# Performance work log

Hardware: AMD Instinct MI355X
Metric: run time of the kernel (lower is better)

## Reference

```python
import jax, jax.numpy as jnp
import numpy as np

B, S, D, H = 2, 2048, 128, 8  # batch, seq, num_hidden(=head dim), num_heads
EPS = 1e-5


def setup_inputs() -> dict:
    key = jax.random.key(0)
    ks = jax.random.split(key, 12)
    sc = 0.02
    return {
        "query": jax.random.normal(ks[0], (B, S, D), dtype=jnp.float32),
        "Wq": jax.random.normal(ks[1], (2 * H * D, D), dtype=jnp.float32) * sc,
        "bq": jnp.zeros((2 * H * D,), dtype=jnp.float32),
        "Wk": jax.random.normal(ks[2], (2 * H * D, D), dtype=jnp.float32) * sc,
        "bk": jnp.zeros((2 * H * D,), dtype=jnp.float32),
        "Wv": jax.random.normal(ks[3], (H * D, D), dtype=jnp.float32) * sc,
        "bv": jnp.zeros((H * D,), dtype=jnp.float32),
        "Wo": jax.random.normal(ks[4], (D, H * D), dtype=jnp.float32) * sc,
        "bo": jnp.zeros((D,), dtype=jnp.float32),
        "gn_w": jnp.ones((H,), dtype=jnp.float32),
        "gn_b": jnp.zeros((H,), dtype=jnp.float32),
        "lam": jax.random.uniform(ks[5], (), dtype=jnp.float32),
    }


def reference(query, Wq, bq, Wk, bk, Wv, bv, Wo, bo, gn_w, gn_b, lam):
    # Faithful to the torch module: the .view calls are raw reshapes (no
    # transpose), d_k=1 so scale is 1, mask=None path (no causal mask),
    # dropout in eval mode, _lambda == _lambda_init == lam.
    q = (query @ Wq.T + bq).reshape(B, H, S, 2 * D)
    k = (query @ Wk.T + bk).reshape(B, H, S, 2 * D)
    v = (query @ Wv.T + bv).reshape(B, H, S, D)
    q1, q2 = q[..., :D], q[..., D:]
    k1, k2 = k[..., :D], k[..., D:]
    s1 = jnp.einsum("bhqd,bhkd->bhqk", q1, k1)  # / sqrt(d_k=1)
    s2 = jnp.einsum("bhqd,bhkd->bhqk", q2, k2)
    attn = jax.nn.softmax(s1, axis=-1) - lam * jax.nn.softmax(s2, axis=-1)
    out = jnp.einsum("bhqk,bhkd->bhqd", attn, v)          # (B,H,S,D)
    out = out.transpose(0, 2, 1, 3).reshape(B, H, S, D)   # faithful raw reshape
    # GroupNorm(num_groups=H, num_channels=H): normalize per (b, h) over (S, D)
    mean = out.mean(axis=(2, 3), keepdims=True)
    var = out.var(axis=(2, 3), keepdims=True)
    out = (out - mean) * jax.lax.rsqrt(var + EPS)
    out = out * gn_w[None, :, None, None] + gn_b[None, :, None, None]
    out = out * (1.0 - lam)
    # torch.cat([out[:, i] for i in range(H)], dim=-1) -> (B, S, H*D)
    out = out.transpose(0, 2, 1, 3).reshape(B, S, H * D)
    return out @ Wo.T + bo
```

## Files before the change

kernel.cpp:

```cpp
#include <hip/hip_runtime.h>

typedef __bf16 bf16x8 __attribute__((ext_vector_type(8)));
typedef __bf16 bf16x4 __attribute__((ext_vector_type(4)));
typedef float  f32x4  __attribute__((ext_vector_type(4)));

#define MFMA16(a,b,c) __builtin_amdgcn_mfma_f32_16x16x32_bf16((a),(b),(c),0,0,0)

__device__ __forceinline__ bf16x8 cvt8(float4 a, float4 b) {
  bf16x8 v;
  v[0]=(__bf16)a.x; v[1]=(__bf16)a.y; v[2]=(__bf16)a.z; v[3]=(__bf16)a.w;
  v[4]=(__bf16)b.x; v[5]=(__bf16)b.y; v[6]=(__bf16)b.z; v[7]=(__bf16)b.w;
  return v;
}
__device__ __forceinline__ bf16x4 cvt4(float4 a) {
  bf16x4 v;
  v[0]=(__bf16)a.x; v[1]=(__bf16)a.y; v[2]=(__bf16)a.z; v[3]=(__bf16)a.w;
  return v;
}


__global__ void to_bf16(const float* __restrict__ q,  const float* __restrict__ wq,
                        const float* __restrict__ wk, const float* __restrict__ wv,
                        const float* __restrict__ wo,
                        __bf16* __restrict__ qb,  __bf16* __restrict__ wqb,
                        __bf16* __restrict__ wkb, __bf16* __restrict__ wvb,
                        __bf16* __restrict__ wob)
{
  const long e = (long)(blockIdx.x * 256 + threadIdx.x) * 8;
  const float* src; __bf16* dst; long off;
  if (e < 524288)       { src = q;  dst = qb;  off = e; }
  else if (e < 786432)  { src = wq; dst = wqb; off = e - 524288; }
  else if (e < 1048576) { src = wk; dst = wkb; off = e - 786432; }
  else if (e < 1179648) { src = wv; dst = wvb; off = e - 1048576; }
  else                  { src = wo; dst = wob; off = e - 1179648; }
  *(bf16x8*)(dst + off) = cvt8(*(const float4*)(src + off), *(const float4*)(src + off + 4));
}

#define LDA 136
__global__ __launch_bounds__(256, 2) void qkv_gemm(
    const __bf16* __restrict__ queryb,
    const __bf16* __restrict__ Wqb, const float* __restrict__ bq,
    const __bf16* __restrict__ Wkb, const float* __restrict__ bk,
    const __bf16* __restrict__ Wvb, const float* __restrict__ bv,
    __bf16* __restrict__ Qbf, __bf16* __restrict__ Kbf, __bf16* __restrict__ Vt)
{
  __shared__ __bf16 As[128 * LDA];
  __shared__ __bf16 Bs[128 * LDA];
  const int t = threadIdx.x;
  const int tile = blockIdx.x;
  const int tm = tile / 40, tn = tile % 40;
  const int m0 = tm * 128, n0 = tn * 128;

  const __bf16* wbase; const float* bias;
  int ocol0; float oscale; int omode;
  if (n0 < 2048)      { wbase = Wqb + n0*128;        bias = bq + n0;        ocol0 = n0;      oscale = 1.4426950408889634f; omode = 0; }
  else if (n0 < 4096) { wbase = Wkb + (n0-2048)*128; bias = bk + (n0-2048); ocol0 = n0-2048; oscale = 1.0f; omode = 1; }
  else                { wbase = Wvb + (n0-4096)*128; bias = bv + (n0-4096); ocol0 = n0-4096; oscale = 1.0f; omode = 2; }

  const __bf16* abase = queryb + (long)m0 * 128;
  for (int r = 0; r < 2; ++r) {
    int e = (r*256 + t) * 32;
    int row = e >> 7, col = e & 127;
    #pragma unroll
    for (int c = 0; c < 4; ++c) {
      *(bf16x8*)&As[row*LDA + col + c*8] = *(const bf16x8*)(abase + (long)row*128 + col + c*8);
      *(bf16x8*)&Bs[row*LDA + col + c*8] = *(const bf16x8*)(wbase + (long)row*128 + col + c*8);
    }
  }
  __syncthreads();

  const int w = t >> 6, lane = t & 63;
  const int lo = lane & 15, quad = lane >> 4;
  const int wm = w >> 1, wn = w & 1;

  f32x4 acc[4][4];
  #pragma unroll
  for (int i = 0; i < 4; ++i)
    #pragma unroll
    for (int j = 0; j < 4; ++j) acc[i][j] = (f32x4){0.f,0.f,0.f,0.f};

  #pragma unroll
  for (int ks = 0; ks < 4; ++ks) {
    bf16x8 af[4], bfr[4];
    #pragma unroll
    for (int i = 0; i < 4; ++i)
      af[i] = *(const bf16x8*)&As[(wm*64 + i*16 + lo)*LDA + ks*32 + quad*8];
    #pragma unroll
    for (int j = 0; j < 4; ++j)
      bfr[j] = *(const bf16x8*)&Bs[(wn*64 + j*16 + lo)*LDA + ks*32 + quad*8];
    #pragma unroll
    for (int i = 0; i < 4; ++i)
      #pragma unroll
      for (int j = 0; j < 4; ++j)
        acc[i][j] = MFMA16(bfr[j], af[i], acc[i][j]);
  }

  if (omode == 2) {
    __syncthreads();
    #pragma unroll
    for (int j = 0; j < 4; ++j) {
      const f32x4 b4 = *(const f32x4*)(bias + wn*64 + j*16 + quad*4);
      #pragma unroll
      for (int i = 0; i < 4; ++i) {
        const int p_l = wm*64 + i*16 + lo;
        #pragma unroll
        for (int r = 0; r < 4; ++r) {
          const int dd_l = wn*64 + j*16 + quad*4 + r;
          As[dd_l*LDA + p_l] = (__bf16)(acc[i][j][r] + b4[r]);
        }
      }
    }
    __syncthreads();
    const int chunkV = ocol0 >> 7;
    __bf16* dst = Vt + (long)(m0 >> 8)*262144 + chunkV*256 + (m0 & 255);
    for (int rr = 0; rr < 8; ++rr) {
      const int unit = rr*256 + t;
      const int dd = unit >> 4, s8 = unit & 15;
      bf16x8 v = *(const bf16x8*)&As[dd*LDA + s8*8];
      *(bf16x8*)(dst + (long)dd*2048 + s8*8) = v;
    }
    return;
  }

  #pragma unroll
  for (int j = 0; j < 4; ++j) {
    const int colb = ocol0 + wn*64 + j*16 + quad*4;
    const f32x4 b4 = *(const f32x4*)(bias + wn*64 + j*16 + quad*4);
    #pragma unroll
    for (int i = 0; i < 4; ++i) {
      const int row = m0 + wm*64 + i*16 + lo;
      bf16x4 v;
      #pragma unroll
      for (int r = 0; r < 4; ++r) v[r] = (__bf16)((acc[i][j][r] + b4[r]) * oscale);
      if (omode == 1) {
        const long flat = (long)(row >> 8)*524288 + (long)(colb >> 8)*65536
                        + (row & 255)*256 + (colb & 255);
        *(bf16x4*)&Kbf[flat] = v;
      } else {
        *(bf16x4*)&Qbf[(long)row*2048 + colb] = v;
      }
    }
  }
}

__global__ __launch_bounds__(256, 2) void attn(
    const __bf16* __restrict__ Qbf, const __bf16* __restrict__ Kbf,
    const __bf16* __restrict__ Vt, __bf16* __restrict__ O,
    const float* __restrict__ lam_p, float* __restrict__ stats)
{
  __shared__ __align__(16) char pool[57344];
  __bf16* Ks  = (__bf16*)pool;
  __bf16* Vs  = (__bf16*)(pool + 32768);
  float*  red = (float*)(pool + 49152);

  const int t = threadIdx.x;
  const int w = t >> 6, lane = t & 63;
  const int lo = lane & 15, quad = lane >> 4;
  const int s = w & 1, qg = w >> 1;
  const int bh = blockIdx.x & 15, qb = blockIdx.x >> 4;
  const float lam = *lam_p;

  const __bf16* Qh = Qbf + (long)bh*524288;
  const __bf16* Kh = Kbf + (long)bh*524288;
  const __bf16* Vh = Vt  + (long)bh*262144;
  const int qrow0 = qb*64 + qg*32;

  bf16x8 qf[2][4];
  #pragma unroll
  for (int qt = 0; qt < 2; ++qt)
    #pragma unroll
    for (int ks = 0; ks < 4; ++ks)
      qf[qt][ks] = *(const bf16x8*)(Qh + (long)(qrow0 + qt*16 + lo)*256 + s*128 + ks*32 + quad*8);

  const int xk = lo & 7;
  int kcolr[4];
  #pragma unroll
  for (int ks = 0; ks < 4; ++ks) kcolr[ks] = ((s*16 + ks*4 + quad) ^ xk) << 3;

  const int vlb = (lo >> 2) * 128;
  const int vc0 = ((4*(lo & 3) + quad) ^ (lo >> 2)) << 3;
  const int vc1 = ((4*(lo & 3) + quad) ^ (lo >> 2) ^ 4) << 3;

  int ke[2], kpos0[2], kpos1[2], vdd[2], vch[2], vpos[2];
  #pragma unroll
  for (int r = 0; r < 2; ++r) {
    ke[r] = (r*256 + t) * 16;
    const int row = ke[r] >> 8;
    const int kcol = ke[r] & 255;
    const int ksrow = (row & 3) + ((row >> 2) & 1)*16 + ((row >> 3) & 3)*4;
    const int sl = kcol >> 3;
    kpos0[r] = ksrow*256 + ((sl       ^ (ksrow & 7)) << 3);
    kpos1[r] = ksrow*256 + (((sl + 1) ^ (ksrow & 7)) << 3);
    const int c = r*256 + t;
    vdd[r] = c >> 2; vch[r] = c & 3;
    const int vrow = vdd[r] >> 2;
    vpos[r] = vrow*128 + ((((vdd[r] & 3) << 2) + vch[r]) ^ (vrow & 7))*8;
  }

  bf16x8 kra[2][2], vra[2];
  #pragma unroll
  for (int r = 0; r < 2; ++r) {
    kra[r][0] = *(const bf16x8*)(Kh + ke[r]);
    kra[r][1] = *(const bf16x8*)(Kh + ke[r] + 8);
    vra[r]    = *(const bf16x8*)(Vh + (long)vdd[r]*2048 + vch[r]*8);
  }
  #pragma unroll
  for (int r = 0; r < 2; ++r) {
    *(bf16x8*)&Ks[kpos0[r]] = kra[r][0];
    *(bf16x8*)&Ks[kpos1[r]] = kra[r][1];
    *(bf16x8*)&Vs[vpos[r]]  = vra[r];
  }

  f32x4 acc[2][8];
  #pragma unroll
  for (int qt = 0; qt < 2; ++qt)
    #pragma unroll
    for (int mt = 0; mt < 8; ++mt) acc[qt][mt] = (f32x4){0.f,0.f,0.f,0.f};
  float lsum[2] = {0.f, 0.f};

  for (int kt = 0; kt < 64; ++kt) {
    __syncthreads();
    if (kt + 1 < 64) {
      #pragma unroll
      for (int r = 0; r < 2; ++r) {
        kra[r][0] = *(const bf16x8*)(Kh + (long)(kt+1)*8192 + ke[r]);
        kra[r][1] = *(const bf16x8*)(Kh + (long)(kt+1)*8192 + ke[r] + 8);
        vra[r]    = *(const bf16x8*)(Vh + (long)vdd[r]*2048 + (kt+1)*32 + vch[r]*8);
      }
    }
    const __bf16* kb = &Ks[(kt & 1) * 8192];
    const __bf16* vb = &Vs[(kt & 1) * 4096];

    f32x4 sf[2][2];
    #pragma unroll
    for (int qt = 0; qt < 2; ++qt)
      #pragma unroll
      for (int nt = 0; nt < 2; ++nt) sf[qt][nt] = (f32x4){0.f,0.f,0.f,0.f};
    #pragma unroll
    for (int nt = 0; nt < 2; ++nt) {
      const int krb = (lo + nt*16) * 256;
      #pragma unroll
      for (int ks = 0; ks < 4; ++ks) {
        bf16x8 kf = *(const bf16x8*)&kb[krb + kcolr[ks]];
        sf[0][nt] = MFMA16(kf, qf[0][ks], sf[0][nt]);
        sf[1][nt] = MFMA16(kf, qf[1][ks], sf[1][nt]);
      }
    }

    bf16x8 pf[2];
    #pragma unroll
    for (int qt = 0; qt < 2; ++qt) {
      #pragma unroll
      for (int nt = 0; nt < 2; ++nt) {
        #pragma unroll
        for (int r = 0; r < 4; ++r) {
          float p = __builtin_exp2f(sf[qt][nt][r]);
          lsum[qt] += p;
          pf[qt][nt*4+r] = (__bf16)p;
        }
      }
    }

    #pragma unroll
    for (int mt = 0; mt < 8; ++mt) {
      bf16x8 vf = *(const bf16x8*)&vb[mt*512 + vlb + ((mt & 1) ? vc1 : vc0)];
      acc[0][mt] = MFMA16(vf, pf[0], acc[0][mt]);
      acc[1][mt] = MFMA16(vf, pf[1], acc[1][mt]);
    }

    if (kt + 1 < 64) {
      __bf16* kn = &Ks[((kt+1) & 1) * 8192];
      __bf16* vn = &Vs[((kt+1) & 1) * 4096];
      #pragma unroll
      for (int r = 0; r < 2; ++r) {
        *(bf16x8*)&kn[kpos0[r]] = kra[r][0];
        *(bf16x8*)&kn[kpos1[r]] = kra[r][1];
        *(bf16x8*)&vn[vpos[r]]  = vra[r];
      }
    }
  }

  #pragma unroll
  for (int qt = 0; qt < 2; ++qt) {
    lsum[qt] += __shfl_xor(lsum[qt], 16);
    lsum[qt] += __shfl_xor(lsum[qt], 32);
  }
  float inv[2];
  const float nume = (s == 0) ? 1.f : lam;
  inv[0] = nume / lsum[0];
  inv[1] = nume / lsum[1];

  float* fs = (float*)pool;
  __syncthreads();
  if (s == 1) {
    #pragma unroll
    for (int qt = 0; qt < 2; ++qt)
      #pragma unroll
      for (int mt = 0; mt < 8; ++mt) {
        f32x4 o;
        #pragma unroll
        for (int r = 0; r < 4; ++r) o[r] = acc[qt][mt][r] * inv[qt];
        *(f32x4*)&fs[(qg*32 + qt*16 + lo)*132 + mt*16 + quad*4] = o;
      }
  }
  __syncthreads();

  float ssum = 0.f, ssq = 0.f;
  if (s == 0) {
    __bf16* Oh = O + (long)bh*262144;
    #pragma unroll
    for (int qt = 0; qt < 2; ++qt)
      #pragma unroll
      for (int mt = 0; mt < 8; ++mt) {
        f32x4 o2 = *(const f32x4*)&fs[(qg*32 + qt*16 + lo)*132 + mt*16 + quad*4];
        bf16x4 ob;
        #pragma unroll
        for (int r = 0; r < 4; ++r) {
          float o = acc[qt][mt][r]*inv[qt] - o2[r];
          ssum += o; ssq += o*o;
          ob[r] = (__bf16)o;
        }
        *(bf16x4*)(Oh + (long)(qrow0 + qt*16 + lo)*128 + mt*16 + quad*4) = ob;
      }
  }
  #pragma unroll
  for (int msk = 1; msk < 64; msk <<= 1) { ssum += __shfl_xor(ssum, msk); ssq += __shfl_xor(ssq, msk); }
  if (lane == 0) { red[w] = ssum; red[4 + w] = ssq; }
  __syncthreads();
  if (t == 0) {
    const int g = (bh >> 3)*8 + (qb >> 2);
    atomicAdd(&stats[g*2],   red[0] + red[1] + red[2] + red[3]);
    atomicAdd(&stats[g*2+1], red[4] + red[5] + red[6] + red[7]);
  }
}

#define LDC 72
__global__ __launch_bounds__(256, 2) void out_gemm(
    const __bf16* __restrict__ O, const float* __restrict__ stats,
    const float* __restrict__ gn_w, const float* __restrict__ gn_b,
    const float* __restrict__ lam_p,
    const __bf16* __restrict__ Wob, const float* __restrict__ bo,
    float* __restrict__ out)
{
  __shared__ __bf16 As[64 * LDC];
  __shared__ __bf16 Bs[128 * LDC];
  const int t = threadIdx.x;
  const int w = t >> 6, lane = t & 63;
  const int lo = lane & 15, quad = lane >> 4;
  const int m0 = (blockIdx.x & 63) * 64;
  const int kq = blockIdx.x >> 6;
  const int b = m0 >> 11;
  const float lam1 = 1.f - *lam_p;

  const int hp = kq;
  const float sN   = stats[(b*8 + hp)*2];
  const float ssN  = stats[(b*8 + hp)*2 + 1];
  const float mean = sN * (1.f/262144.f);
  const float rstd = rsqrtf(ssN * (1.f/262144.f) - mean*mean + 1e-5f);
  const float gwv  = gn_w[hp] * rstd * lam1;
  const float shv  = (gn_b[hp] - mean * rstd * gn_w[hp]) * lam1;

  f32x4 acc[8];
  #pragma unroll
  for (int j = 0; j < 8; ++j) acc[j] = (f32x4){0.f,0.f,0.f,0.f};

  for (int kc = 0; kc < 2; ++kc) {
    const int k0 = kq*128 + kc*64;
    const int d0 = kc*64;
    __syncthreads();
    for (int r = 0; r < 4; ++r) {
      int e = r*1024 + t*4;
      int row_l = e >> 6, col_l = e & 63;
      const int spp = (m0 + row_l) & 2047;
      const int h = spp & 7, srow = hp*256 + (spp >> 3);
      bf16x4 v = *(const bf16x4*)(O + ((long)(b*8 + h)*2048 + srow)*128 + d0 + col_l);
      bf16x4 o;
      #pragma unroll
      for (int q = 0; q < 4; ++q) o[q] = (__bf16)((float)v[q]*gwv + shv);
      *(bf16x4*)&As[row_l*LDC + col_l] = o;
    }
    for (int r = 0; r < 8; ++r) {
      int e = (r*256 + t) * 4;
      int row = e >> 6, col = e & 63;
      *(bf16x4*)&Bs[row*LDC + col] = *(const bf16x4*)(Wob + (long)row*1024 + k0 + col);
    }
    __syncthreads();
    #pragma unroll
    for (int ks = 0; ks < 2; ++ks) {
      bf16x8 af = *(const bf16x8*)&As[(w*16 + lo)*LDC + ks*32 + quad*8];
      #pragma unroll
      for (int j = 0; j < 8; ++j) {
        bf16x8 bfr = *(const bf16x8*)&Bs[(j*16 + lo)*LDC + ks*32 + quad*8];
        acc[j] = MFMA16(af, bfr, acc[j]);
      }
    }
  }
  #pragma unroll
  for (int j = 0; j < 8; ++j) {
    const int col = j*16 + lo;
    const float bb = bo[col] * 0.125f;
    #pragma unroll
    for (int r = 0; r < 4; ++r)
      atomicAdd(&out[(long)(m0 + w*16 + quad*4 + r)*128 + col], acc[j][r] + bb);
  }
}

extern "C" void kernel_launch(void* const* d_in, const int* in_sizes, int n_in,
                              void* d_out, int out_size, void* d_ws, size_t ws_size,
                              hipStream_t stream) {
  const float* query = (const float*)d_in[0];
  const float* Wq = (const float*)d_in[1];
  const float* bq = (const float*)d_in[2];
  const float* Wk = (const float*)d_in[3];
  const float* bk = (const float*)d_in[4];
  const float* Wv = (const float*)d_in[5];
  const float* bv = (const float*)d_in[6];
  const float* Wo = (const float*)d_in[7];
  const float* bo = (const float*)d_in[8];
  const float* gn_w = (const float*)d_in[9];
  const float* gn_b = (const float*)d_in[10];
  const float* lam = (const float*)d_in[11];

  char* ws = (char*)d_ws;
  __bf16* Qbf   = (__bf16*)(ws);
  __bf16* Kbf   = (__bf16*)(ws + (16l<<20));
  __bf16* Vt    = (__bf16*)(ws + (40l<<20));
  __bf16* O     = (__bf16*)(ws + (48l<<20));
  __bf16* queryb= (__bf16*)(ws + (64l<<20));
  __bf16* Wqb   = (__bf16*)(ws + (65l<<20));
  __bf16* Wkb   = (__bf16*)(ws + (65l<<20) + (512l<<10));
  __bf16* Wvb   = (__bf16*)(ws + (66l<<20));
  __bf16* Wob   = (__bf16*)(ws + (66l<<20) + (256l<<10));
  float*  stats = (float* )(ws + (66l<<20) + (512l<<10));
  float* out = (float*)d_out;

  to_bf16 <<<dim3(640),  dim3(256), 0, stream>>>(query, Wq, Wk, Wv, Wo,
                                                 queryb, Wqb, Wkb, Wvb, Wob);
  qkv_gemm<<<dim3(1280), dim3(256), 0, stream>>>(queryb, Wqb, bq, Wkb, bk, Wvb, bv, Qbf, Kbf, Vt);
  attn    <<<dim3(512),  dim3(256), 0, stream>>>(Qbf, Kbf, Vt, O, lam, stats);
  out_gemm<<<dim3(512),  dim3(256), 0, stream>>>(O, stats, gn_w, gn_b, lam, Wob, bo, out);
}
```

Before: 204.4 us.

## Store V pre-swizzled in MFMA fragment order and load it directly into registers

The V projection epilogue now writes V in the exact per-lane MFMA operand layout, tiled by key block and M tile. The attention kernel then loads each lane's V fragments straight from global memory into double-buffered registers, with the loop unrolled by two. This removes the V staging through shared memory and its LDS reads and writes. The cost is more live registers (16 bf16x8 vectors), which may reduce occupancy or cause spills under the launch bound of 2 blocks.

```diff
diff --git a/kernel.cpp b/kernel.cpp
--- a/kernel.cpp
+++ b/kernel.cpp
@@ -112,12 +112,16 @@
     }
     __syncthreads();
     const int chunkV = ocol0 >> 7;
-    __bf16* dst = Vt + (long)(m0 >> 8)*262144 + chunkV*256 + (m0 & 255);
+    const int ktbase = chunkV*8 + ((m0 & 255) >> 5);
+    __bf16* dst = Vt + (long)(m0 >> 8)*262144;
     for (int rr = 0; rr < 8; ++rr) {
-      const int unit = rr*256 + t;
-      const int dd = unit >> 4, s8 = unit & 15;
-      bf16x8 v = *(const bf16x8*)&As[dd*LDA + s8*8];
-      *(bf16x8*)(dst + (long)dd*2048 + s8*8) = v;
+      const int u = rr*256 + t;
+      const int kt_l = u >> 9;
+      const int mt   = (u >> 6) & 7;
+      const int lane_v = u & 63;
+      const int qv = (u >> 4) & 3, lov = u & 15;
+      bf16x8 v = *(const bf16x8*)&As[(mt*16 + lov)*LDA + kt_l*32 + qv*8];
+      *(bf16x8*)(dst + (long)(ktbase + kt_l)*4096 + mt*512 + lane_v*8) = v;
     }
     return;
   }
@@ -150,7 +154,6 @@
 {
   __shared__ __align__(16) char pool[57344];
   __bf16* Ks  = (__bf16*)pool;
-  __bf16* Vs  = (__bf16*)(pool + 32768);
   float*  red = (float*)(pool + 49152);
 
   const int t = threadIdx.x;
@@ -162,7 +165,7 @@
 
   const __bf16* Qh = Qbf + (long)bh*524288;
   const __bf16* Kh = Kbf + (long)bh*524288;
-  const __bf16* Vh = Vt  + (long)bh*262144;
+  const __bf16* Vh = Vt  + (long)bh*262144 + lane*8;
   const int qrow0 = qb*64 + qg*32;
 
   bf16x8 qf[2][4];
@@ -177,11 +180,7 @@
   #pragma unroll
   for (int ks = 0; ks < 4; ++ks) kcolr[ks] = ((s*16 + ks*4 + quad) ^ xk) << 3;
 
-  const int vlb = (lo >> 2) * 128;
-  const int vc0 = ((4*(lo & 3) + quad) ^ (lo >> 2)) << 3;
-  const int vc1 = ((4*(lo & 3) + quad) ^ (lo >> 2) ^ 4) << 3;
-
-  int ke[2], kpos0[2], kpos1[2], vdd[2], vch[2], vpos[2];
+  int ke[2], kpos0[2], kpos1[2];
   #pragma unroll
   for (int r = 0; r < 2; ++r) {
     ke[r] = (r*256 + t) * 16;
@@ -191,25 +190,23 @@
     const int sl = kcol >> 3;
     kpos0[r] = ksrow*256 + ((sl       ^ (ksrow & 7)) << 3);
     kpos1[r] = ksrow*256 + (((sl + 1) ^ (ksrow & 7)) << 3);
-    const int c = r*256 + t;
-    vdd[r] = c >> 2; vch[r] = c & 3;
-    const int vrow = vdd[r] >> 2;
-    vpos[r] = vrow*128 + ((((vdd[r] & 3) << 2) + vch[r]) ^ (vrow & 7))*8;
-  }
-
-  bf16x8 kra[2][2], vra[2];
+  }
+
+  bf16x8 kra[2][2];
   #pragma unroll
   for (int r = 0; r < 2; ++r) {
     kra[r][0] = *(const bf16x8*)(Kh + ke[r]);
     kra[r][1] = *(const bf16x8*)(Kh + ke[r] + 8);
-    vra[r]    = *(const bf16x8*)(Vh + (long)vdd[r]*2048 + vch[r]*8);
   }
   #pragma unroll
   for (int r = 0; r < 2; ++r) {
     *(bf16x8*)&Ks[kpos0[r]] = kra[r][0];
     *(bf16x8*)&Ks[kpos1[r]] = kra[r][1];
-    *(bf16x8*)&Vs[vpos[r]]  = vra[r];
-  }
+  }
+
+  bf16x8 vfA[8], vfB[8];
+  #pragma unroll
+  for (int mt = 0; mt < 8; ++mt) vfA[mt] = *(const bf16x8*)(Vh + mt*512);
 
   f32x4 acc[2][8];
   #pragma unroll
@@ -218,67 +215,69 @@
     for (int mt = 0; mt < 8; ++mt) acc[qt][mt] = (f32x4){0.f,0.f,0.f,0.f};
   float lsum[2] = {0.f, 0.f};
 
-  for (int kt = 0; kt < 64; ++kt) {
-    __syncthreads();
-    if (kt + 1 < 64) {
-      #pragma unroll
-      for (int r = 0; r < 2; ++r) {
-        kra[r][0] = *(const bf16x8*)(Kh + (long)(kt+1)*8192 + ke[r]);
-        kra[r][1] = *(const bf16x8*)(Kh + (long)(kt+1)*8192 + ke[r] + 8);
-        vra[r]    = *(const bf16x8*)(Vh + (long)vdd[r]*2048 + (kt+1)*32 + vch[r]*8);
-      }
-    }
-    const __bf16* kb = &Ks[(kt & 1) * 8192];
-    const __bf16* vb = &Vs[(kt & 1) * 4096];
-
-    f32x4 sf[2][2];
-    #pragma unroll
-    for (int qt = 0; qt < 2; ++qt)
-      #pragma unroll
-      for (int nt = 0; nt < 2; ++nt) sf[qt][nt] = (f32x4){0.f,0.f,0.f,0.f};
-    #pragma unroll
-    for (int nt = 0; nt < 2; ++nt) {
-      const int krb = (lo + nt*16) * 256;
-      #pragma unroll
-      for (int ks = 0; ks < 4; ++ks) {
-        bf16x8 kf = *(const bf16x8*)&kb[krb + kcolr[ks]];
-        sf[0][nt] = MFMA16(kf, qf[0][ks], sf[0][nt]);
-        sf[1][nt] = MFMA16(kf, qf[1][ks], sf[1][nt]);
-      }
-    }
-
-    bf16x8 pf[2];
-    #pragma unroll
-    for (int qt = 0; qt < 2; ++qt) {
-      #pragma unroll
-      for (int nt = 0; nt < 2; ++nt) {
-        #pragma unroll
-        for (int r = 0; r < 4; ++r) {
-          float p = __builtin_exp2f(sf[qt][nt][r]);
-          lsum[qt] += p;
-          pf[qt][nt*4+r] = (__bf16)p;
-        }
-      }
-    }
-
-    #pragma unroll
-    for (int mt = 0; mt < 8; ++mt) {
-      bf16x8 vf = *(const bf16x8*)&vb[mt*512 + vlb + ((mt & 1) ? vc1 : vc0)];
-      acc[0][mt] = MFMA16(vf, pf[0], acc[0][mt]);
-      acc[1][mt] = MFMA16(vf, pf[1], acc[1][mt]);
-    }
-
-    if (kt + 1 < 64) {
-      __bf16* kn = &Ks[((kt+1) & 1) * 8192];
-      __bf16* vn = &Vs[((kt+1) & 1) * 4096];
-      #pragma unroll
-      for (int r = 0; r < 2; ++r) {
-        *(bf16x8*)&kn[kpos0[r]] = kra[r][0];
-        *(bf16x8*)&kn[kpos1[r]] = kra[r][1];
-        *(bf16x8*)&vn[vpos[r]]  = vra[r];
-      }
-    }
-  }
+#define BODY(KT, VFC, VFN)                                                   \
+  {                                                                          \
+    __syncthreads();                                                         \
+    const int ktn = (KT) + 1;                                                \
+    if (ktn < 64) {                                                          \
+      _Pragma("unroll")                                                      \
+      for (int r = 0; r < 2; ++r) {                                          \
+        kra[r][0] = *(const bf16x8*)(Kh + (long)ktn*8192 + ke[r]);           \
+        kra[r][1] = *(const bf16x8*)(Kh + (long)ktn*8192 + ke[r] + 8);       \
+      }                                                                      \
+      _Pragma("unroll")                                                      \
+      for (int mt = 0; mt < 8; ++mt)                                         \
+        VFN[mt] = *(const bf16x8*)(Vh + (long)ktn*4096 + mt*512);            \
+    }                                                                        \
+    const __bf16* kb = &Ks[((KT) & 1) * 8192];                               \
+    f32x4 sf[2][2];                                                          \
+    _Pragma("unroll")                                                        \
+    for (int qt = 0; qt < 2; ++qt)                                           \
+      _Pragma("unroll")                                                      \
+      for (int nt = 0; nt < 2; ++nt) sf[qt][nt] = (f32x4){0.f,0.f,0.f,0.f};  \
+    _Pragma("unroll")                                                        \
+    for (int nt = 0; nt < 2; ++nt) {                                         \
+      const int krb = (lo + nt*16) * 256;                                    \
+      _Pragma("unroll")                                                      \
+      for (int ks = 0; ks < 4; ++ks) {                                       \
+        bf16x8 kf = *(const bf16x8*)&kb[krb + kcolr[ks]];                    \
+        sf[0][nt] = MFMA16(kf, qf[0][ks], sf[0][nt]);                        \
+        sf[1][nt] = MFMA16(kf, qf[1][ks], sf[1][nt]);                        \
+      }                                                                      \
+    }                                                                        \
+    bf16x8 pf[2];                                                            \
+    _Pragma("unroll")                                                        \
+    for (int qt = 0; qt < 2; ++qt) {                                         \
+      _Pragma("unroll")                                                      \
+      for (int nt = 0; nt < 2; ++nt) {                                       \
+        _Pragma("unroll")                                                    \
+        for (int r = 0; r < 4; ++r) {                                        \
+          float p = __builtin_exp2f(sf[qt][nt][r]);                          \
+          lsum[qt] += p;                                                     \
+          pf[qt][nt*4+r] = (__bf16)p;                                        \
+        }                                                                    \
+      }                                                                      \
+    }                                                                        \
+    _Pragma("unroll")                                                        \
+    for (int mt = 0; mt < 8; ++mt) {                                         \
+      acc[0][mt] = MFMA16(VFC[mt], pf[0], acc[0][mt]);                       \
+      acc[1][mt] = MFMA16(VFC[mt], pf[1], acc[1][mt]);                       \
+    }                                                                        \
+    if (ktn < 64) {                                                          \
+      __bf16* kn = &Ks[(ktn & 1) * 8192];                                    \
+      _Pragma("unroll")                                                      \
+      for (int r = 0; r < 2; ++r) {                                          \
+        *(bf16x8*)&kn[kpos0[r]] = kra[r][0];                                 \
+        *(bf16x8*)&kn[kpos1[r]] = kra[r][1];                                 \
+      }                                                                      \
+    }                                                                        \
+  }
+
+  for (int kt = 0; kt < 64; kt += 2) {
+    BODY(kt,     vfA, vfB);
+    BODY(kt + 1, vfB, vfA);
+  }
+#undef BODY
 
   #pragma unroll
   for (int qt = 0; qt < 2; ++qt) {
```

After: 212.2 us. +3.8%, slower.
